# Optimization experiments

Hardware: AMD Instinct MI355X
Metric: run time of the kernel (lower is better)

The kernel has to match this reference:

```python
import jax, jax.numpy as jnp
import numpy as np

B, C, T, V = 64, 64, 128, 25   # batch, in_channels, frames, joints
R = 8                          # rel_channels = in_channels // rel_reduction
TS = 9                         # time_step (temporal taps of dynamic adjacency)
OUT = 64                       # out_channels (conv3)


def setup_inputs() -> dict:
    key = jax.random.key(0)
    ks = jax.random.split(key, 10)
    p = lambda k, shape: jax.random.normal(k, shape, jnp.float32) * 0.05
    return {
        'x':  jax.random.normal(ks[0], (B, C, T, V), jnp.float32),
        'A':  jax.random.normal(ks[1], (V, V), jnp.float32) * 0.1,
        'W1': p(ks[2], (R, C)),       'b1': p(ks[3], (R,)),
        'W2': p(ks[4], (R, C)),       'b2': p(ks[5], (R,)),
        'W4': p(ks[6], (C * TS, R)),  'b4': p(ks[7], (C * TS,)),
        'W3': p(ks[8], (OUT, C)),     'b3': p(ks[9], (OUT,)),
    }


def reference(x, A, W1, b1, W2, b2, W4, b4, W3, b3):
    alpha = 1.0
    # conv1/conv2: 1x1 Conv2d then mean over time (dim -2). 1x1 conv is linear,
    # so mean(conv(x)) == einsum/T + bias.  -> (B, R, V)
    x1 = jnp.einsum('rc,bctv->brv', W1, x) / T + b1[None, :, None]
    x2 = jnp.einsum('rc,bctv->brv', W2, x) / T + b2[None, :, None]
    # tanh relation: (B, R, V, 1) - (B, R, 1, V) -> (B, R, V, V)
    rel = jnp.tanh(x1[:, :, :, None] - x2[:, :, None, :])
    # conv4 (1x1): rel_channels -> C*TS dynamic adjacency, + static A
    Adyn = jnp.einsum('or,brij->boij', W4, rel) + b4[None, :, None, None]
    Adyn = Adyn * alpha + A[None, None]                      # (B, C*TS, V, V)
    # reshape(B, C, TS, V, V).permute(0,1,3,4,2): per-(b,c) temporal graph kernel
    Wk = Adyn.reshape(B, C, TS, V, V).transpose(0, 1, 3, 4, 2)  # (B, C, V, V, TS)
    # x -> (B, C, V, T), causal left-pad by TS-1 (matches F.pad(x, (TS-1, 0)))
    xp = jnp.pad(x.transpose(0, 1, 3, 2), ((0, 0), (0, 0), (0, 0), (TS - 1, 0)))
    # Grouped conv1d loop over V vertices, fused into TS tap-wise einsums:
    # z[b,c,t,i] = sum_{v,k} xp[b,c,v,t+k] * Wk[b,c,v,i,k]   (stride=1)
    z = jnp.zeros((B, C, T, V), x.dtype)
    for k in range(TS):  # small fixed tap loop
        z = z + jnp.einsum('bcvt,bcvi->bcti', xp[..., k:k + T], Wk[..., k])
    # conv3: 1x1 Conv2d C -> OUT
    out = jnp.einsum('oc,bctv->botv', W3, z) + b3[None, :, None, None]
    return out
```

## Files before the change

kernel.cpp:

```cpp
#include <hip/hip_runtime.h>
#include <hip/hip_bf16.h>

#define BB 64
#define CC 64
#define TT_ 128
#define VV 25
#define RR 8
#define TS_ 9
#define OO 64

typedef __hip_bfloat16 bf16;
typedef __attribute__((ext_vector_type(8))) short short8;
typedef __attribute__((ext_vector_type(4))) float f32x4;

__device__ __forceinline__ unsigned short f2b(float f) {
    bf16 h = __float2bfloat16(f);
    return __builtin_bit_cast(unsigned short, h);
}

__global__ __launch_bounds__(256) void k_mean(const float* __restrict__ x,
                                              float* __restrict__ xm) {
    __shared__ float sm[256];
    int bc = blockIdx.x;
    int tid = threadIdx.x;
    const float* p = x + (size_t)bc * TT_ * VV;
    float s = 0.f;
    if (tid < 250) {
        for (int off = tid; off < TT_ * VV; off += 250) s += p[off];
    }
    sm[tid] = s;
    __syncthreads();
    if (tid < VV) {
        float tot = 0.f;
        #pragma unroll
        for (int g = 0; g < 10; g++) tot += sm[g * VV + tid];
        xm[bc * VV + tid] = tot * (1.0f / TT_);
    }
}

__global__ __launch_bounds__(256) void k_rel(const float* __restrict__ xm,
                                             const float* __restrict__ W1,
                                             const float* __restrict__ b1,
                                             const float* __restrict__ W2,
                                             const float* __restrict__ b2,
                                             float* __restrict__ rel) {
    __shared__ float x1s[RR][VV];
    __shared__ float x2s[RR][VV];
    int b = blockIdx.x, tid = threadIdx.x;
    for (int idx = tid; idx < RR * VV; idx += 256) {
        int r = idx / VV, v = idx % VV;
        float s1 = b1[r], s2 = b2[r];
        for (int c = 0; c < CC; c++) {
            float xv = xm[(b * CC + c) * VV + v];
            s1 += W1[r * CC + c] * xv;
            s2 += W2[r * CC + c] * xv;
        }
        x1s[r][v] = s1;
        x2s[r][v] = s2;
    }
    __syncthreads();
    float* relb = rel + (size_t)b * VV * VV * RR;
    for (int idx = tid; idx < VV * VV * RR; idx += 256) {
        int r = idx % RR;
        int i = (idx / RR) % VV;
        int v = idx / (RR * VV);
        relb[idx] = tanhf(x1s[r][v] - x2s[r][i]);
    }
}

__global__ __launch_bounds__(256) void k_z(const float* __restrict__ x,
                                           const float* __restrict__ Ag,
                                           const float* __restrict__ W4,
                                           const float* __restrict__ b4,
                                           const float* __restrict__ rel,
                                           bf16* __restrict__ zws) {
    __shared__ __align__(16) unsigned short xpadB[136 * 40];
    __shared__ __align__(16) unsigned short AdbS[TS_ * 32 * 40];

    int tid = threadIdx.x;
    int bc = blockIdx.x;
    int b = bc / CC, c = bc % CC;

    if (tid < 128) ((unsigned int*)xpadB)[(tid >> 4) * 20 + (tid & 15)] = 0u;
    for (int id = tid; id < 128 * 7; id += 256) {
        int r = 8 + id / 7, v = 25 + id % 7;
        xpadB[r * 40 + v] = 0;
    }
    for (int id = tid; id < TS_ * 25 * 7; id += 256) {
        int s = id / 175, rem = id % 175;
        int i = rem / 7, v = 25 + rem % 7;
        AdbS[(s * 32 + i) * 40 + v] = 0;
    }
    const float4* xg4 = (const float4*)(x + (size_t)bc * TT_ * VV);
    for (int i4 = tid; i4 < TT_ * VV / 4; i4 += 256) {
        float4 f = xg4[i4];
        int idx = i4 * 4;
        float fe[4] = {f.x, f.y, f.z, f.w};
        #pragma unroll
        for (int e = 0; e < 4; e++) {
            int t = (idx + e) / VV, v = (idx + e) % VV;
            xpadB[(t + 8) * 40 + v] = f2b(fe[e]);
        }
    }

    const float* relb = rel + (size_t)b * VV * VV * RR;
    const float* W4c = W4 + c * TS_ * RR;
    const float* b4c = b4 + c * TS_;
    for (int task = tid; task < VV * VV; task += 256) {
        int v = task / VV, i = task % VV;
        const float4* r4 = (const float4*)(relb + (size_t)task * RR);
        float4 ra = r4[0], rb_ = r4[1];
        float av = Ag[task];
        #pragma unroll
        for (int s = 0; s < TS_; s++) {
            float a2 = b4c[s] + av;
            a2 += W4c[s*8+0] * ra.x  + W4c[s*8+1] * ra.y
                + W4c[s*8+2] * ra.z  + W4c[s*8+3] * ra.w;
            a2 += W4c[s*8+4] * rb_.x + W4c[s*8+5] * rb_.y
                + W4c[s*8+6] * rb_.z + W4c[s*8+7] * rb_.w;
            AdbS[(s * 32 + i) * 40 + v] = f2b(a2);
        }
    }
    __syncthreads();

    int lane = tid & 63, wv = tid >> 6;
    int ml = lane & 15, qd = lane >> 4;
    f32x4 acc00 = {0.f, 0.f, 0.f, 0.f};
    f32x4 acc01 = acc00, acc10 = acc00, acc11 = acc00;
    int rowA0 = (wv * 2) * 16 + ml;
    #pragma unroll
    for (int s = 0; s < TS_; s++) {
        short8 a0 = *(const short8*)&xpadB[(rowA0 + s) * 40 + qd * 8];
        short8 a1 = *(const short8*)&xpadB[(rowA0 + 16 + s) * 40 + qd * 8];
        short8 b0 = *(const short8*)&AdbS[(s * 32 + ml) * 40 + qd * 8];
        short8 b1 = *(const short8*)&AdbS[(s * 32 + 16 + ml) * 40 + qd * 8];
        acc00 = __builtin_amdgcn_mfma_f32_16x16x32_bf16(a0, b0, acc00, 0, 0, 0);
        acc01 = __builtin_amdgcn_mfma_f32_16x16x32_bf16(a0, b1, acc01, 0, 0, 0);
        acc10 = __builtin_amdgcn_mfma_f32_16x16x32_bf16(a1, b0, acc10, 0, 0, 0);
        acc11 = __builtin_amdgcn_mfma_f32_16x16x32_bf16(a1, b1, acc11, 0, 0, 0);
    }

    bf16* zb = zws + (size_t)bc * TT_ * VV;
    int t0 = (wv * 2) * 16 + qd * 4;
    int i0 = ml, i1 = 16 + ml;
    #pragma unroll
    for (int r = 0; r < 4; r++) {
        zb[(t0 + r) * VV + i0]      = __float2bfloat16(acc00[r]);
        zb[(t0 + 16 + r) * VV + i0] = __float2bfloat16(acc10[r]);
    }
    if (i1 < VV) {
        #pragma unroll
        for (int r = 0; r < 4; r++) {
            zb[(t0 + r) * VV + i1]      = __float2bfloat16(acc01[r]);
            zb[(t0 + 16 + r) * VV + i1] = __float2bfloat16(acc11[r]);
        }
    }
}

__global__ __launch_bounds__(256) void k_conv3(const bf16* __restrict__ zws,
                                               const float* __restrict__ W3,
                                               const float* __restrict__ b3,
                                               float* __restrict__ out) {
    __shared__ __align__(16) unsigned short w3b[OO * 72];
    __shared__ __align__(16) unsigned short zl[CC * 130];
    __shared__ float b3l[OO];
    int tid = threadIdx.x;
    int b = blockIdx.x / 25, tile = blockIdx.x % 25;
    int tj0 = tile * 128;

    if (tid < OO) b3l[tid] = b3[tid];
    for (int idx = tid; idx < OO * CC; idx += 256) {
        int o = idx >> 6, c = idx & 63;
        w3b[o * 72 + c] = f2b(W3[idx]);
    }
    const unsigned int* zg = (const unsigned int*)(zws + (size_t)b * CC * (TT_ * VV));
    for (int idu = tid; idu < CC * 64; idu += 256) {
        int c = idu >> 6, ju = idu & 63;
        ((unsigned int*)zl)[c * 65 + ju] = zg[c * 1600 + (tj0 >> 1) + ju];
    }
    __syncthreads();

    int lane = tid & 63, wv = tid >> 6;
    int ml = lane & 15, qd = lane >> 4;
    f32x4 acc[4][2];
    #pragma unroll
    for (int m = 0; m < 4; m++)
        #pragma unroll
        for (int nl = 0; nl < 2; nl++) acc[m][nl] = (f32x4){0.f, 0.f, 0.f, 0.f};

    #pragma unroll
    for (int k0 = 0; k0 < 2; k0++) {
        short8 a[4];
        #pragma unroll
        for (int m = 0; m < 4; m++)
            a[m] = *(const short8*)&w3b[(m * 16 + ml) * 72 + k0 * 32 + qd * 8];
        #pragma unroll
        for (int nl = 0; nl < 2; nl++) {
            int col = (2 * wv + nl) * 16 + ml;
            int cb = k0 * 32 + qd * 8;
            short8 bf;
            #pragma unroll
            for (int j = 0; j < 8; j++)
                bf[j] = (short)zl[(cb + j) * 130 + col];
            #pragma unroll
            for (int m = 0; m < 4; m++)
                acc[m][nl] = __builtin_amdgcn_mfma_f32_16x16x32_bf16(a[m], bf, acc[m][nl], 0, 0, 0);
        }
    }

    float* ob = out + (size_t)b * OO * (TT_ * VV) + tj0;
    #pragma unroll
    for (int m = 0; m < 4; m++)
        #pragma unroll
        for (int nl = 0; nl < 2; nl++) {
            int col = (2 * wv + nl) * 16 + ml;
            #pragma unroll
            for (int r = 0; r < 4; r++) {
                int o = m * 16 + qd * 4 + r;
                ob[(size_t)o * (TT_ * VV) + col] = acc[m][nl][r] + b3l[o];
            }
        }
}

extern "C" void kernel_launch(void* const* d_in, const int* in_sizes, int n_in,
                              void* d_out, int out_size, void* d_ws, size_t ws_size,
                              hipStream_t stream) {
    const float* x  = (const float*)d_in[0];
    const float* A  = (const float*)d_in[1];
    const float* W1 = (const float*)d_in[2];
    const float* b1 = (const float*)d_in[3];
    const float* W2 = (const float*)d_in[4];
    const float* b2 = (const float*)d_in[5];
    const float* W4 = (const float*)d_in[6];
    const float* b4 = (const float*)d_in[7];
    const float* W3 = (const float*)d_in[8];
    const float* b3 = (const float*)d_in[9];
    float* out = (float*)d_out;

    char* ws = (char*)d_ws;
    float* xm   = (float*)(ws);
    float* rel  = (float*)(ws + 409600);
    bf16*  zws  = (bf16*)(ws + 1689600);

    k_mean <<<BB * CC, 256, 0, stream>>>(x, xm);
    k_rel  <<<BB,      256, 0, stream>>>(xm, W1, b1, W2, b2, rel);
    k_z    <<<BB * CC, 256, 0, stream>>>(x, A, W4, b4, rel, zws);
    k_conv3<<<BB * 25, 256, 0, stream>>>(zws, W3, b3, out);
}
```

Baseline: 172.4 us.

## Vectorize loads in mean, conv3 weight staging; cache xm in shared; simplify index math

k_mean now reads x with float4 loads and four independent partial sums per thread, then reduces 32 partials per joint. k_rel stages the per-batch means into shared memory before the channel reduction. k_z replaces per-element div/mod with incremental index updates when unpacking x, and k_conv3 converts W3 with float4 loads and packed 4-wide bf16 shared stores. These are small independent memory-access and index-arithmetic tweaks spread across several kernels, aimed at prologue and staging overhead.

New measurement: 163.4 us. 5.2% less time.

```diff
diff --git a/kernel.cpp b/kernel.cpp
--- a/kernel.cpp
+++ b/kernel.cpp
@@ -11,6 +11,7 @@
 
 typedef __hip_bfloat16 bf16;
 typedef __attribute__((ext_vector_type(8))) short short8;
+typedef __attribute__((ext_vector_type(4))) short s16x4;
 typedef __attribute__((ext_vector_type(4))) float f32x4;
 
 __device__ __forceinline__ unsigned short f2b(float f) {
@@ -20,20 +21,27 @@
 
 __global__ __launch_bounds__(256) void k_mean(const float* __restrict__ x,
                                               float* __restrict__ xm) {
-    __shared__ float sm[256];
+    __shared__ float smf[800];
     int bc = blockIdx.x;
     int tid = threadIdx.x;
-    const float* p = x + (size_t)bc * TT_ * VV;
-    float s = 0.f;
-    if (tid < 250) {
-        for (int off = tid; off < TT_ * VV; off += 250) s += p[off];
-    }
-    sm[tid] = s;
+    const float4* p4 = (const float4*)(x + (size_t)bc * TT_ * VV);
+    if (tid < 200) {
+        float4 a = p4[tid];
+        float4 b = p4[tid + 200];
+        float4 c = p4[tid + 400];
+        float4 d = p4[tid + 600];
+        float4 s;
+        s.x = a.x + b.x + c.x + d.x;
+        s.y = a.y + b.y + c.y + d.y;
+        s.z = a.z + b.z + c.z + d.z;
+        s.w = a.w + b.w + c.w + d.w;
+        ((float4*)smf)[tid] = s;
+    }
     __syncthreads();
     if (tid < VV) {
         float tot = 0.f;
         #pragma unroll
-        for (int g = 0; g < 10; g++) tot += sm[g * VV + tid];
+        for (int m = 0; m < 32; m++) tot += smf[tid + VV * m];
         xm[bc * VV + tid] = tot * (1.0f / TT_);
     }
 }
@@ -44,14 +52,17 @@
                                              const float* __restrict__ W2,
                                              const float* __restrict__ b2,
                                              float* __restrict__ rel) {
+    __shared__ float xms[CC * VV];
     __shared__ float x1s[RR][VV];
     __shared__ float x2s[RR][VV];
     int b = blockIdx.x, tid = threadIdx.x;
+    for (int i = tid; i < CC * VV; i += 256) xms[i] = xm[b * CC * VV + i];
+    __syncthreads();
     for (int idx = tid; idx < RR * VV; idx += 256) {
         int r = idx / VV, v = idx % VV;
         float s1 = b1[r], s2 = b2[r];
         for (int c = 0; c < CC; c++) {
-            float xv = xm[(b * CC + c) * VV + v];
+            float xv = xms[c * VV + v];
             s1 += W1[r * CC + c] * xv;
             s2 += W2[r * CC + c] * xv;
         }
@@ -95,11 +106,13 @@
     for (int i4 = tid; i4 < TT_ * VV / 4; i4 += 256) {
         float4 f = xg4[i4];
         int idx = i4 * 4;
+        int t = idx / VV, v = idx - t * VV;
         float fe[4] = {f.x, f.y, f.z, f.w};
         #pragma unroll
         for (int e = 0; e < 4; e++) {
-            int t = (idx + e) / VV, v = (idx + e) % VV;
             xpadB[(t + 8) * 40 + v] = f2b(fe[e]);
+            v++;
+            if (v == VV) { v = 0; t++; }
         }
     }
 
@@ -169,9 +182,16 @@
     int tj0 = tile * 128;
 
     if (tid < OO) b3l[tid] = b3[tid];
-    for (int idx = tid; idx < OO * CC; idx += 256) {
-        int o = idx >> 6, c = idx & 63;
-        w3b[o * 72 + c] = f2b(W3[idx]);
+    const float4* W3v = (const float4*)W3;
+    for (int idx = tid; idx < OO * CC / 4; idx += 256) {
+        float4 f = W3v[idx];
+        int o = idx >> 4, c4 = (idx & 15) * 4;
+        s16x4 s4;
+        s4[0] = (short)f2b(f.x);
+        s4[1] = (short)f2b(f.y);
+        s4[2] = (short)f2b(f.z);
+        s4[3] = (short)f2b(f.w);
+        *(s16x4*)&w3b[o * 72 + c4] = s4;
     }
     const unsigned int* zg = (const unsigned int*)(zws + (size_t)b * CC * (TT_ * VV));
     for (int idu = tid; idu < CC * 64; idu += 256) {
```
